# Performance work log

Measured on AMD Instinct MI355X. Metric: run time of the kernel, lower is better.

The kernel has to match this reference:

```python
import jax, jax.numpy as jnp
import numpy as np

TOKENS = 8192
MODEL_DIM = 4096
PROMPT_DIM = 64
NUM_EXPERTS = 8
TOP_K = 2
EPS = float(np.finfo(np.float32).eps)


def setup_inputs() -> dict:
    key = jax.random.key(0)
    k1, k2, k3 = jax.random.split(key, 3)
    x = jax.random.normal(k1, (TOKENS, MODEL_DIM), dtype=jnp.float32)
    prompt = jax.random.normal(k2, (TOKENS, PROMPT_DIM), dtype=jnp.float32)
    # gate linear: Linear(model_dim + prompt_dim, num_experts, bias=True)
    W = jax.random.normal(k3, (MODEL_DIM + PROMPT_DIM, NUM_EXPERTS), dtype=jnp.float32) * 0.02
    b = jnp.zeros((NUM_EXPERTS,), dtype=jnp.float32)
    return {"x": x, "prompt": prompt, "W": W, "b": b}


def reference(x, prompt, W, b):
    # eval path: no jitter, no noise (self.training is False)
    logits = jnp.concatenate([x, prompt], axis=-1) @ W + b          # [T, E]
    _, topk_idx = jax.lax.top_k(logits, TOP_K)                      # [T, K]
    masks = jax.nn.one_hot(topk_idx, NUM_EXPERTS, dtype=jnp.float32)  # [T, K, E]
    gates = jax.nn.softmax(logits, axis=-1)                         # [T, E]
    gates_s = jnp.einsum("te,tke->tk", gates, masks)               # masked gather-sum
    if TOP_K > 1:
        denom = jnp.maximum(gates_s.sum(axis=-1, keepdims=True), EPS)
        gates_s = gates_s / denom
    # masks[:, i] == masks_se[i], gates_s[:, i] == gates_s[i] in the torch code
    return masks, gates_s
```

## Files before the change

kernel.cpp:

```cpp
#include <hip/hip_runtime.h>
#include <math.h>

#define NE 8
#define TPW 4
#define TOKENS_PER_BLOCK 16
#define EPS_F32 1.1920929e-07f

__device__ __forceinline__ void fma8(float xs, const float4& lo, const float4& hi, float* a) {
    a[0] = fmaf(xs, lo.x, a[0]);
    a[1] = fmaf(xs, lo.y, a[1]);
    a[2] = fmaf(xs, lo.z, a[2]);
    a[3] = fmaf(xs, lo.w, a[3]);
    a[4] = fmaf(xs, hi.x, a[4]);
    a[5] = fmaf(xs, hi.y, a[5]);
    a[6] = fmaf(xs, hi.z, a[6]);
    a[7] = fmaf(xs, hi.w, a[7]);
}

__global__ __launch_bounds__(256, 2)
void topk_gate(const float* __restrict__ x,
               const float* __restrict__ prompt,
               const float* __restrict__ W,
               const float* __restrict__ b,
               float* __restrict__ out,
               int tokens)
{
    const int lane = threadIdx.x & 63;
    const int wave = threadIdx.x >> 6;
    const int tbase = blockIdx.x * TOKENS_PER_BLOCK + wave * TPW;

    float acc[TPW][NE];
#pragma unroll
    for (int t = 0; t < TPW; ++t)
#pragma unroll
        for (int e = 0; e < NE; ++e) acc[t][e] = 0.f;

#pragma unroll 2
    for (int i = 0; i < 16; ++i) {
        const int k = i * 256 + lane * 4;
        float4 wlo[4], whi[4];
#pragma unroll
        for (int j = 0; j < 4; ++j) {
            wlo[j] = *(const float4*)(W + (size_t)(k + j) * 8);
            whi[j] = *(const float4*)(W + (size_t)(k + j) * 8 + 4);
        }
#pragma unroll
        for (int t = 0; t < TPW; ++t) {
            const float4 xv = *(const float4*)(x + (size_t)(tbase + t) * 4096 + k);
            fma8(xv.x, wlo[0], whi[0], acc[t]);
            fma8(xv.y, wlo[1], whi[1], acc[t]);
            fma8(xv.z, wlo[2], whi[2], acc[t]);
            fma8(xv.w, wlo[3], whi[3], acc[t]);
        }
    }

    if (lane < 16) {
        const int k = lane * 4;
        float4 wlo[4], whi[4];
#pragma unroll
        for (int j = 0; j < 4; ++j) {
            wlo[j] = *(const float4*)(W + (size_t)(4096 + k + j) * 8);
            whi[j] = *(const float4*)(W + (size_t)(4096 + k + j) * 8 + 4);
        }
#pragma unroll
        for (int t = 0; t < TPW; ++t) {
            const float4 pv = *(const float4*)(prompt + (size_t)(tbase + t) * 64 + k);
            fma8(pv.x, wlo[0], whi[0], acc[t]);
            fma8(pv.y, wlo[1], whi[1], acc[t]);
            fma8(pv.z, wlo[2], whi[2], acc[t]);
            fma8(pv.w, wlo[3], whi[3], acc[t]);
        }
    }

#pragma unroll
    for (int t = 0; t < TPW; ++t)
#pragma unroll
        for (int e = 0; e < NE; ++e) {
            float v = acc[t][e];
#pragma unroll
            for (int off = 32; off >= 1; off >>= 1)
                v += __shfl_xor(v, off, 64);
            acc[t][e] = v;
        }

    const int tt = lane >> 4;
    const int kk = (lane >> 3) & 1;
    const int ee = lane & 7;

    float lg[NE];
#pragma unroll
    for (int e = 0; e < NE; ++e) {
        float v = acc[0][e];
        if (tt == 1) v = acc[1][e];
        if (tt == 2) v = acc[2][e];
        if (tt == 3) v = acc[3][e];
        lg[e] = v + b[e];
    }

    float v0 = lg[0]; int i0 = 0;
#pragma unroll
    for (int e = 1; e < NE; ++e)
        if (lg[e] > v0) { v0 = lg[e]; i0 = e; }
    float v1 = (i0 == 0) ? lg[1] : lg[0];
    int   i1 = (i0 == 0) ? 1 : 0;
#pragma unroll
    for (int e = 0; e < NE; ++e) {
        if (e != i0 && lg[e] > v1) { v1 = lg[e]; i1 = e; }
    }

    float s = 0.f;
#pragma unroll
    for (int e = 0; e < NE; ++e) s += __expf(lg[e] - v0);
    const float g0 = 1.0f / s;
    const float g1 = __expf(v1 - v0) / s;
    const float denom = fmaxf(g0 + g1, EPS_F32);

    const int sel = kk ? i1 : i0;
    const int t_global = tbase + tt;
    out[(size_t)t_global * 16 + kk * 8 + ee] = (ee == sel) ? 1.0f : 0.0f;

    if ((lane & 15) < 2) {
        const float g = (ee == 0) ? (g0 / denom) : (g1 / denom);
        out[(size_t)tokens * 16 + (size_t)t_global * 2 + ee] = g;
    }
}

extern "C" void kernel_launch(void* const* d_in, const int* in_sizes, int n_in,
                              void* d_out, int out_size, void* d_ws, size_t ws_size,
                              hipStream_t stream) {
    const float* x      = (const float*)d_in[0];
    const float* prompt = (const float*)d_in[1];
    const float* W      = (const float*)d_in[2];
    const float* b      = (const float*)d_in[3];
    float* out          = (float*)d_out;

    const int tokens = in_sizes[0] / 4096;
    const int grid   = tokens / TOKENS_PER_BLOCK;

    hipLaunchKernelGGL(topk_gate, dim3(grid), dim3(256), 0, stream,
                       x, prompt, W, b, out, tokens);
}
```

Baseline: 223.3 us.

## Split K across wave pairs with LDS reduction and smaller token blocks

```diff
diff --git a/kernel.cpp b/kernel.cpp
--- a/kernel.cpp
+++ b/kernel.cpp
@@ -2,8 +2,6 @@
 #include <math.h>
 
 #define NE 8
-#define TPW 4
-#define TOKENS_PER_BLOCK 16
 #define EPS_F32 1.1920929e-07f
 
 __device__ __forceinline__ void fma8(float xs, const float4& lo, const float4& hi, float* a) {
@@ -17,7 +15,7 @@
     a[7] = fmaf(xs, hi.w, a[7]);
 }
 
-__global__ __launch_bounds__(256, 2)
+__global__ __launch_bounds__(256, 4)
 void topk_gate(const float* __restrict__ x,
                const float* __restrict__ prompt,
                const float* __restrict__ W,
@@ -25,37 +23,55 @@
                float* __restrict__ out,
                int tokens)
 {
-    const int lane = threadIdx.x & 63;
-    const int wave = threadIdx.x >> 6;
-    const int tbase = blockIdx.x * TOKENS_PER_BLOCK + wave * TPW;
+    const int tid  = threadIdx.x;
+    const int lane = tid & 63;
+    const int wave = tid >> 6;
+    const int pair = wave >> 1;
+    const int ks   = wave & 1;
+    const int tblock = blockIdx.x * 8;
+    const int tbase  = tblock + pair * 4;
 
-    float acc[TPW][NE];
+    __shared__ float lds[2][2][4][NE];
+
+    float acc[4][NE];
 #pragma unroll
-    for (int t = 0; t < TPW; ++t)
+    for (int t = 0; t < 4; ++t)
 #pragma unroll
         for (int e = 0; e < NE; ++e) acc[t][e] = 0.f;
 
+    const int kofs = ks * 2048;
+
 #pragma unroll 2
-    for (int i = 0; i < 16; ++i) {
-        const int k = i * 256 + lane * 4;
+    for (int i = 0; i < 8; ++i) {
+        const int k = kofs + i * 256 + lane * 4;
+
+        float4 xv[4];
+#pragma unroll
+        for (int t = 0; t < 4; ++t)
+            xv[t] = *(const float4*)(x + (size_t)(tbase + t) * 4096 + k);
+
         float4 wlo[4], whi[4];
 #pragma unroll
         for (int j = 0; j < 4; ++j) {
             wlo[j] = *(const float4*)(W + (size_t)(k + j) * 8);
             whi[j] = *(const float4*)(W + (size_t)(k + j) * 8 + 4);
         }
+
 #pragma unroll
-        for (int t = 0; t < TPW; ++t) {
-            const float4 xv = *(const float4*)(x + (size_t)(tbase + t) * 4096 + k);
-            fma8(xv.x, wlo[0], whi[0], acc[t]);
-            fma8(xv.y, wlo[1], whi[1], acc[t]);
-            fma8(xv.z, wlo[2], whi[2], acc[t]);
-            fma8(xv.w, wlo[3], whi[3], acc[t]);
+        for (int t = 0; t < 4; ++t) {
+            fma8(xv[t].x, wlo[0], whi[0], acc[t]);
+            fma8(xv[t].y, wlo[1], whi[1], acc[t]);
+            fma8(xv[t].z, wlo[2], whi[2], acc[t]);
+            fma8(xv[t].w, wlo[3], whi[3], acc[t]);
         }
     }
 
-    if (lane < 16) {
+    if (ks == 1 && lane < 16) {
         const int k = lane * 4;
+        float4 pv[4];
+#pragma unroll
+        for (int t = 0; t < 4; ++t)
+            pv[t] = *(const float4*)(prompt + (size_t)(tbase + t) * 64 + k);
         float4 wlo[4], whi[4];
 #pragma unroll
         for (int j = 0; j < 4; ++j) {
@@ -63,17 +79,16 @@
             whi[j] = *(const float4*)(W + (size_t)(4096 + k + j) * 8 + 4);
         }
 #pragma unroll
-        for (int t = 0; t < TPW; ++t) {
-            const float4 pv = *(const float4*)(prompt + (size_t)(tbase + t) * 64 + k);
-            fma8(pv.x, wlo[0], whi[0], acc[t]);
-            fma8(pv.y, wlo[1], whi[1], acc[t]);
-            fma8(pv.z, wlo[2], whi[2], acc[t]);
-            fma8(pv.w, wlo[3], whi[3], acc[t]);
+        for (int t = 0; t < 4; ++t) {
+            fma8(pv[t].x, wlo[0], whi[0], acc[t]);
+            fma8(pv[t].y, wlo[1], whi[1], acc[t]);
+            fma8(pv[t].z, wlo[2], whi[2], acc[t]);
+            fma8(pv[t].w, wlo[3], whi[3], acc[t]);
         }
     }
 
 #pragma unroll
-    for (int t = 0; t < TPW; ++t)
+    for (int t = 0; t < 4; ++t)
 #pragma unroll
         for (int e = 0; e < NE; ++e) {
             float v = acc[t][e];
@@ -83,45 +98,50 @@
             acc[t][e] = v;
         }
 
-    const int tt = lane >> 4;
-    const int kk = (lane >> 3) & 1;
-    const int ee = lane & 7;
+    if (lane < 32) {
+        const int t = lane >> 3;
+        const int e = lane & 7;
+        lds[pair][ks][t][e] = acc[t][e];
+    }
+    __syncthreads();
 
-    float lg[NE];
+    if (tid < 128) {
+        const int tl = tid >> 4;
+        const int kk = (tid >> 3) & 1;
+        const int ee = tid & 7;
+        const int p  = tl >> 2;
+        const int t4 = tl & 3;
+
+        float lg[NE];
 #pragma unroll
-    for (int e = 0; e < NE; ++e) {
-        float v = acc[0][e];
-        if (tt == 1) v = acc[1][e];
-        if (tt == 2) v = acc[2][e];
-        if (tt == 3) v = acc[3][e];
-        lg[e] = v + b[e];
-    }
+        for (int e = 0; e < NE; ++e)
+            lg[e] = lds[p][0][t4][e] + lds[p][1][t4][e] + b[e];
 
-    float v0 = lg[0]; int i0 = 0;
+        float v0 = lg[0]; int i0 = 0;
 #pragma unroll
-    for (int e = 1; e < NE; ++e)
-        if (lg[e] > v0) { v0 = lg[e]; i0 = e; }
-    float v1 = (i0 == 0) ? lg[1] : lg[0];
-    int   i1 = (i0 == 0) ? 1 : 0;
+        for (int e = 1; e < NE; ++e)
+            if (lg[e] > v0) { v0 = lg[e]; i0 = e; }
+        float v1 = (i0 == 0) ? lg[1] : lg[0];
+        int   i1 = (i0 == 0) ? 1 : 0;
 #pragma unroll
-    for (int e = 0; e < NE; ++e) {
-        if (e != i0 && lg[e] > v1) { v1 = lg[e]; i1 = e; }
-    }
+        for (int e = 0; e < NE; ++e)
+            if (e != i0 && lg[e] > v1) { v1 = lg[e]; i1 = e; }
 
-    float s = 0.f;
+        float s = 0.f;
 #pragma unroll
-    for (int e = 0; e < NE; ++e) s += __expf(lg[e] - v0);
-    const float g0 = 1.0f / s;
-    const float g1 = __expf(v1 - v0) / s;
-    const float denom = fmaxf(g0 + g1, EPS_F32);
+        for (int e = 0; e < NE; ++e) s += __expf(lg[e] - v0);
+        const float g0 = 1.0f / s;
+        const float g1 = __expf(v1 - v0) / s;
+        const float denom = fmaxf(g0 + g1, EPS_F32);
 
-    const int sel = kk ? i1 : i0;
-    const int t_global = tbase + tt;
-    out[(size_t)t_global * 16 + kk * 8 + ee] = (ee == sel) ? 1.0f : 0.0f;
+        const int t_global = tblock + tl;
+        const int sel = kk ? i1 : i0;
+        out[(size_t)t_global * 16 + kk * 8 + ee] = (ee == sel) ? 1.0f : 0.0f;
 
-    if ((lane & 15) < 2) {
-        const float g = (ee == 0) ? (g0 / denom) : (g1 / denom);
-        out[(size_t)tokens * 16 + (size_t)t_global * 2 + ee] = g;
+        if ((tid & 15) < 2) {
+            const float g = (ee == 0) ? (g0 / denom) : (g1 / denom);
+            out[(size_t)tokens * 16 + (size_t)t_global * 2 + ee] = g;
+        }
     }
 }
 
@@ -135,7 +155,7 @@
     float* out          = (float*)d_out;
 
     const int tokens = in_sizes[0] / 4096;
-    const int grid   = tokens / TOKENS_PER_BLOCK;
+    const int grid   = tokens / 8;
 
     hipLaunchKernelGGL(topk_gate, dim3(grid), dim3(256), 0, stream,
                        x, prompt, W, b, out, tokens);
```

After: 244.9 us. +9.7%, slower.
